# Kernel tuning notes

Hardware: AMD Instinct MI355X
Metric: run time of the kernel (lower is better)

## Reference

```python
import jax, jax.numpy as jnp
import numpy as np

HEAD_DIM = 128
N_HEADS = 16
N_KV_HEADS = 4
ROPE_BASE = 10000.0
TRAIN_SEQ_LEN = 1024


def _rotary_cos_sin(seq_len, rd, base=ROPE_BASE, train_len=TRAIN_SEQ_LEN):
    # NTK-style base scaling when seq_len exceeds training length (matches Rotary.forward)
    if seq_len > train_len:
        scale = seq_len / train_len
        base = base * scale ** (rd / (rd - 2))
    inv_freq = 1.0 / base ** (np.arange(0, rd, 2, dtype=np.float32) / rd)
    freqs = np.outer(np.arange(seq_len, dtype=np.float32), inv_freq)  # [T, rd/2]
    cos = jnp.asarray(np.cos(freqs))[None, :, None, :]  # [1,T,1,rd/2]
    sin = jnp.asarray(np.sin(freqs))[None, :, None, :]
    return cos, sin


def _apply_rotary(x, cos, sin):
    h = x.shape[-1] // 2
    x1, x2 = x[..., :h], x[..., h:]
    return jnp.concatenate((x1 * cos + x2 * sin, -x1 * sin + x2 * cos), axis=-1)


def _rms_norm(x):
    eps = jnp.finfo(x.dtype).eps
    return x * jax.lax.rsqrt(jnp.mean(x * x, axis=-1, keepdims=True) + eps)


def setup_inputs() -> dict:
    key = jax.random.key(0)
    ks = jax.random.split(key, 6)
    B, T, D = 4, 2048, 2048
    x = jax.random.normal(ks[0], (B, T, D), dtype=jnp.float32)
    q_w = jax.random.normal(ks[1], (D, D), dtype=jnp.float32) * 0.02
    k_w = jax.random.normal(ks[2], (N_KV_HEADS * HEAD_DIM, D), dtype=jnp.float32) * 0.02
    v_w = jax.random.normal(ks[3], (N_KV_HEADS * HEAD_DIM, D), dtype=jnp.float32) * 0.02
    out_w = jax.random.normal(ks[4], (D, D), dtype=jnp.float32) * 0.02
    q_gain = jnp.ones((N_HEADS,), dtype=jnp.float32)
    return {"x": x, "q_w": q_w, "k_w": k_w, "v_w": v_w, "out_w": out_w, "q_gain": q_gain}


def reference(x, q_w, k_w, v_w, out_w, q_gain):
    B, T, D = x.shape
    q = (x @ q_w.T).reshape(B, T, N_HEADS, HEAD_DIM)
    k = (x @ k_w.T).reshape(B, T, N_KV_HEADS, HEAD_DIM)
    v = (x @ v_w.T).reshape(B, T, N_KV_HEADS, HEAD_DIM)
    q = _rms_norm(q)
    k = _rms_norm(k)
    cos, sin = _rotary_cos_sin(T, HEAD_DIM)
    q = _apply_rotary(q, cos, sin)
    k = _apply_rotary(k, cos, sin)
    q = q * q_gain[None, None, :, None]
    # GQA: expand kv heads (repeat_interleave semantics)
    rep = N_HEADS // N_KV_HEADS
    k = jnp.repeat(k, rep, axis=2)  # [B,T,H,D]
    v = jnp.repeat(v, rep, axis=2)
    scale = 1.0 / jnp.sqrt(jnp.asarray(HEAD_DIM, dtype=x.dtype))
    scores = jnp.einsum("bthd,bshd->bhts", q, k) * scale  # [B,H,T,T]
    causal = jnp.tril(jnp.ones((T, T), dtype=bool))
    scores = jnp.where(causal[None, None], scores, jnp.asarray(-jnp.inf, dtype=scores.dtype))
    w = jax.nn.softmax(scores, axis=-1)
    y = jnp.einsum("bhts,bshd->bthd", w, v).reshape(B, T, D)
    return y @ out_w.T
```

## Files before the change

### kernel.cpp

```cpp
#include <hip/hip_runtime.h>
#include <hip/hip_bf16.h>
#include <math.h>

#define HEAD_DIM 128
#define NH 16
#define NKV 4
#define BB 4
#define TT 2048
#define DD 2048
#define ROWS (BB*TT)

typedef unsigned short u16;
typedef unsigned int u32;
typedef __attribute__((ext_vector_type(8))) short short8;
typedef __attribute__((ext_vector_type(4))) float f32x4;
typedef __attribute__((ext_vector_type(16))) float f32x16;
typedef __attribute__((ext_vector_type(4))) unsigned short u16x4;

__device__ __forceinline__ float bf2f(u16 u) {
    union { unsigned int i; float f; } v; v.i = ((unsigned int)u) << 16; return v.f;
}
__device__ __forceinline__ u16 f2bf(float f) {
    union { float f; unsigned int i; } v; v.f = f;
    unsigned int r = v.i + 0x7FFFu + ((v.i >> 16) & 1u);
    return (u16)(r >> 16);
}
__device__ __forceinline__ f32x4 mfma16(short8 a, short8 b, f32x4 c) {
    return __builtin_amdgcn_mfma_f32_16x16x32_bf16(a, b, c, 0, 0, 0);
}
__device__ __forceinline__ f32x16 mfma32(short8 a, short8 b, f32x16 c) {
    return __builtin_amdgcn_mfma_f32_32x32x16_bf16(a, b, c, 0, 0, 0);
}
__device__ __forceinline__ f32x16 zero16() {
    f32x16 z;
    #pragma unroll
    for (int i = 0; i < 16; ++i) z[i] = 0.f;
    return z;
}
__device__ __forceinline__ void gload_lds16(const u16* g, u16* l) {
    __builtin_amdgcn_global_load_lds(
        (const __attribute__((address_space(1))) unsigned int*)(const void*)g,
        (__attribute__((address_space(3))) unsigned int*)(void*)l, 16, 0, 0);
}

__global__ __launch_bounds__(256)
void cast_f2b(const float* __restrict__ in, u16* __restrict__ out, int n)
{
    int i = (blockIdx.x * 256 + threadIdx.x) * 4;
    if (i >= n) return;
    float4 v = *(const float4*)(in + i);
    u16x4 o;
    o.x = f2bf(v.x); o.y = f2bf(v.y); o.z = f2bf(v.z); o.w = f2bf(v.w);
    *(u16x4*)(out + i) = o;
}

__global__ __launch_bounds__(256)
void prep_all(const float* __restrict__ x,  const float* __restrict__ qw,
              const float* __restrict__ kw, const float* __restrict__ vw,
              u16* __restrict__ xh, u16* __restrict__ wq, u16* __restrict__ wkv,
              float* __restrict__ cs, float* __restrict__ sn, float base)
{
    const int bid = blockIdx.x, tid = threadIdx.x;
    if (bid < 22528) {
        const float* src; u16* dst; int i4;
        if (bid < 16384)      { src = x;  dst = xh;            i4 = bid; }
        else if (bid < 20480) { src = qw; dst = wq;            i4 = bid - 16384; }
        else if (bid < 21504) { src = kw; dst = wkv;           i4 = bid - 20480; }
        else                  { src = vw; dst = wkv + 1048576; i4 = bid - 21504; }
        int i = (i4 * 256 + tid) * 4;
        float4 v = *(const float4*)(src + i);
        u16x4 o;
        o.x = f2bf(v.x); o.y = f2bf(v.y); o.z = f2bf(v.z); o.w = f2bf(v.w);
        *(u16x4*)(dst + i) = o;
    } else {
        int idx = (bid - 22528) * 256 + tid;
        int t = idx >> 6;
        int d = idx & 63;
        float inv = powf(base, -(float)(2 * d) / 128.0f);
        float f = (float)t * inv;
        cs[idx] = cosf(f);
        sn[idx] = sinf(f);
    }
}

__global__ __launch_bounds__(256)
void rmsrope_qk(const u16* __restrict__ qin, u16* __restrict__ qout,
                const u16* __restrict__ kin, u16* __restrict__ kout,
                const float* __restrict__ cs, const float* __restrict__ sn,
                const float* __restrict__ gain, float pre)
{
    int row  = blockIdx.x * 4 + (threadIdx.x >> 6);
    int lane = threadIdx.x & 63;
    const u16* xin; u16* xout; int heads; int use_gain;
    if (row < 131072) { xin = qin; xout = qout; heads = NH;  use_gain = 1; }
    else { row -= 131072; xin = kin; xout = kout; heads = NKV; use_gain = 0; }

    int h = row % heads;
    int t = (row / heads) % TT;
    int b = row / (heads * TT);
    size_t base = (size_t)row * HEAD_DIM;

    float x1 = bf2f(xin[base + lane]);
    float x2 = bf2f(xin[base + 64 + lane]);
    float ss = x1 * x1 + x2 * x2;
    #pragma unroll
    for (int m = 1; m < 64; m <<= 1) ss += __shfl_xor(ss, m, 64);
    float r = 1.0f / sqrtf(ss * (1.0f / 128.0f) + 1.1920929e-7f);
    x1 *= r; x2 *= r;

    float c = cs[t * 64 + lane];
    float s = sn[t * 64 + lane];
    float o1 =  x1 * c + x2 * s;
    float o2 = -x1 * s + x2 * c;
    float g = use_gain ? gain[h] * pre : 1.0f;
    o1 *= g; o2 *= g;

    size_t obase = ((size_t)(b * heads + h) * TT + t) * HEAD_DIM;
    xout[obase + lane]      = f2bf(o1);
    xout[obase + 64 + lane] = f2bf(o2);
}

__global__ __launch_bounds__(256)
void transpose_v(const u16* __restrict__ vbh, u16* __restrict__ vtb)
{
    __shared__ u16 tile[64][72];
    const int tb = blockIdx.x;
    const int db = blockIdx.y;
    const int z  = blockIdx.z;
    const int tid = threadIdx.x;

    {
        const int r = tid >> 2, cq = tid & 3;
        const u16* src = vbh + ((size_t)(((z >> 2) * TT + tb * 64 + r) * NKV + (z & 3))) * 128
                             + db * 64 + cq * 16;
        short8 s0 = *(const short8*)(src);
        short8 s1 = *(const short8*)(src + 8);
        #pragma unroll
        for (int e = 0; e < 8; ++e) tile[r][cq * 16 + e]     = (u16)s0[e];
        #pragma unroll
        for (int e = 0; e < 8; ++e) tile[r][cq * 16 + 8 + e] = (u16)s1[e];
    }
    __syncthreads();
    {
        const int d = tid >> 2, tq = tid & 3;
        __attribute__((aligned(16))) u16 tmp[16];
        #pragma unroll
        for (int e = 0; e < 16; ++e) {
            int esw = (e & 3) | ((e & 4) << 1) | ((e & 8) >> 1);
            tmp[e] = tile[tq * 16 + esw][d];
        }
        u16* dst = vtb + (((size_t)(z * (TT / 64) + tb) * 128 + (db * 64 + d)) << 6) + tq * 16;
        *(short8*)(dst)     = ((short8*)tmp)[0];
        *(short8*)(dst + 8) = ((short8*)tmp)[1];
    }
}

template<int BN, int OUTMODE>
__global__ __launch_bounds__(512, 2)
void gemm256(const u16* __restrict__ A, const u16* __restrict__ W,
             void* __restrict__ C0, void* __restrict__ C1)
{
    constexpr int WN    = (BN == 256) ? 4 : 2;
    constexpr int MR    = (BN == 256) ? 8 : 4;
    constexpr int WROW  = (BN == 256) ? 128 : 64;
    constexpr int NT    = DD / 64;
    constexpr int NBI   = (BN == 256) ? 4 : 2;
    constexpr int BPR   = BN / 16;

    __shared__ u16 AsL[2 * 128 * 128];
    __shared__ u16 BsL[2 * (BN / 2) * 128];

    const int tid = threadIdx.x;
    const int w = tid >> 6, l = tid & 63;
    const int lq = l & 15, lg = l >> 4;
    const int wmi = (WN == 4) ? (w >> 2) : (w >> 1);
    const int wni = w & (WN - 1);

    int bmi, bni;
    {
        const int bid = blockIdx.x;
        const int wg = (bid & 7) * 32 + (bid >> 3);
        const int st = wg >> 2, wi = wg & 3;
        const int sty = st >> 2, stx = st & 3;
        bmi = sty * 2 + (wi >> 1);
        bni = stx * 2 + (wi & 1);
    }
    const int bm = bmi * 256, bn = bni * BN;

    const int sro = l >> 4;
    const int sch = l & 15;

    f32x4 acc[MR][4];
    #pragma unroll
    for (int m = 0; m < MR; ++m)
        #pragma unroll
        for (int n = 0; n < 4; ++n) acc[m][n] = (f32x4){0.f, 0.f, 0.f, 0.f};

    auto stage = [&](int buf, int t) {
        const size_t ko = (size_t)t * 64;
        u16* Ad = AsL + buf * (128 * 128);
        u16* Bd = BsL + buf * ((BN / 2) * 128);
        #pragma unroll
        for (int j = 0; j < 4; ++j) {
            int rp = w * 16 + j * 4 + sro;
            int cg = sch ^ (rp & 15);
            gload_lds16(A + (size_t)(bm + 2 * rp + (cg >> 3)) * DD + ko + (cg & 7) * 8,
                        Ad + (w * 16 + j * 4) * 128);
        }
        #pragma unroll
        for (int j = 0; j < NBI; ++j) {
            int rp = w * BPR + j * 4 + sro;
            int cg = sch ^ (rp & 15);
            gload_lds16(W + (size_t)(bn + 2 * rp + (cg >> 3)) * DD + ko + (cg & 7) * 8,
                        Bd + (w * BPR + j * 4) * 128);
        }
    };

    stage(0, 0);
    stage(1, 1);
    if constexpr (BN == 256) asm volatile("s_waitcnt vmcnt(8)" ::: "memory");
    else                     asm volatile("s_waitcnt vmcnt(6)" ::: "memory");
    __builtin_amdgcn_s_barrier();
    __builtin_amdgcn_sched_barrier(0);

    const int mh = lq >> 1;
    const int e8 = (lq & 1) << 3;
    for (int t = 0; t < NT; ++t) {
        const int buf = t & 1;
        const u16* Ab = AsL + buf * (128 * 128);
        const u16* Bb = BsL + buf * ((BN / 2) * 128);
        #pragma unroll
        for (int ks = 0; ks < 2; ++ks) {
            short8 af[MR], bf[4];
            #pragma unroll
            for (int m = 0; m < MR; ++m) {
                int rp = wmi * (WROW / 2) + m * 8 + mh;
                af[m] = *(const short8*)(Ab + rp * 128 + (((e8 + ks * 4 + lg) ^ (rp & 15)) << 3));
            }
            #pragma unroll
            for (int n = 0; n < 4; ++n) {
                int rp = wni * 32 + n * 8 + mh;
                bf[n] = *(const short8*)(Bb + rp * 128 + (((e8 + ks * 4 + lg) ^ (rp & 15)) << 3));
            }
            __builtin_amdgcn_s_setprio(1);
            #pragma unroll
            for (int m = 0; m < MR; ++m)
                #pragma unroll
                for (int n = 0; n < 4; ++n)
                    acc[m][n] = mfma16(af[m], bf[n], acc[m][n]);
            __builtin_amdgcn_s_setprio(0);
        }

        if (t + 1 < NT) {
            __builtin_amdgcn_sched_barrier(0);
            __builtin_amdgcn_s_barrier();
            if (t + 2 < NT) {
                stage(buf, t + 2);
                if constexpr (BN == 256) asm volatile("s_waitcnt vmcnt(8)" ::: "memory");
                else                     asm volatile("s_waitcnt vmcnt(6)" ::: "memory");
            } else {
                asm volatile("s_waitcnt vmcnt(0)" ::: "memory");
            }
            __builtin_amdgcn_s_barrier();
            __builtin_amdgcn_sched_barrier(0);
        }
    }

    #pragma unroll
    for (int m = 0; m < MR; ++m) {
        int grow = bm + wmi * WROW + m * 16 + lg * 4;
        #pragma unroll
        for (int n = 0; n < 4; ++n) {
            int col = wni * 64 + n * 16 + lq;
            #pragma unroll
            for (int q = 0; q < 4; ++q) {
                float v = acc[m][n][q];
                if constexpr (OUTMODE == 0) {
                    ((u16*)C0)[(size_t)(grow + q) * 2048 + bn + col] = f2bf(v);
                } else if constexpr (OUTMODE == 2) {
                    ((float*)C0)[(size_t)(grow + q) * 2048 + bn + col] = v;
                } else {
                    int cg = bn + col;
                    if (cg < 512)
                        ((u16*)C0)[(size_t)(grow + q) * 512 + cg] = f2bf(v);
                    else
                        ((u16*)C1)[(size_t)(grow + q) * 512 + (cg - 512)] = f2bf(v);
                }
            }
        }
    }
}

__global__ __launch_bounds__(256, 2)
void attn_mfma(const u16* __restrict__ qg,
               const u16* __restrict__ kg,
               const u16* __restrict__ vtg,
               u16* __restrict__ yg)
{
    __shared__ u16 Ks[2][64 * 128];
    __shared__ u16 Vs[2][64 * 128];

    const int tid = threadIdx.x, wid = tid >> 6, l = tid & 63;
    const int lq = l & 31, hi = l >> 5, hi4 = hi << 2;

    const int bid = blockIdx.x;
    const int xcd  = bid & 7;
    const int s    = bid >> 3;
    const int gsub = s >> 5;
    const int hh   = (s >> 3) & 3;
    const int fold = s & 7;
    const int g    = xcd + (gsub << 3);
    const int b = g >> 2, kvh = g & 3;
    const int h = kvh * 4 + hh;

    const u16* kg_bh = kg + (((size_t)g * TT) << 7);
    const u16* vt_bh = vtg + (size_t)g * (TT / 64) * 8192;
    const u16* q_bh  = qg + (((size_t)(b * NH + h) * TT) << 7);

    const int nta = 2 * fold + 2;
    const int NT  = 34;

    const int sro = l >> 4;
    const int sch = l & 15;

    auto stage = [&](int buf, int kt) {
        #pragma unroll
        for (int i = 0; i < 4; ++i) {
            int kr = wid * 16 + i * 4 + sro;
            int cgk = sch ^ (kr & 15);
            gload_lds16(kg_bh + (((size_t)(kt * 64 + kr)) << 7) + (cgk << 3),
                        &Ks[buf][(wid * 16 + i * 4) << 7]);
            int rp = wid * 16 + i * 4 + sro;
            int cgv = sch ^ (rp & 15);
            gload_lds16(vt_bh + (size_t)kt * 8192 + ((2 * rp + (cgv >> 3)) << 6) + ((cgv & 7) << 3),
                        &Vs[buf][(wid * 16 + i * 4) << 7]);
        }
    };

    stage(0, 0);
    stage(1, 1);
    asm volatile("s_waitcnt vmcnt(8)" ::: "memory");
    __builtin_amdgcn_s_barrier();
    __builtin_amdgcn_sched_barrier(0);

    int step = 0;

    for (int seg = 0; seg < 2; ++seg) {
        const int qblk = seg ? (15 - fold) : fold;
        const int nseg = seg ? (32 - 2 * fold) : nta;
        const int qrow = qblk * 128 + wid * 32 + lq;
        const int diag = (qblk * 128 + wid * 32) >> 6;

        const u16* qptr = q_bh + ((size_t)qrow << 7) + hi * 8;
        short8 qf[8];
        #pragma unroll
        for (int q = 0; q < 8; ++q)
            qf[q] = *(const short8*)(qptr + q * 16);

        f32x16 accO[4];
        #pragma unroll
        for (int d = 0; d < 4; ++d) accO[d] = zero16();
        float m2 = -1e30f, lr = 0.f;

        for (int kt = 0; kt < nseg; ++kt, ++step) {
            const int buf = step & 1;

            if (kt <= diag) {
                const u16* Kc = Ks[buf];
                f32x16 accS0 = zero16(), accS1 = zero16();
                __builtin_amdgcn_s_setprio(1);
                #pragma unroll
                for (int ss = 0; ss < 8; ++ss) {
                    int c = ((2 * ss + hi) ^ (lq & 15)) << 3;
                    short8 kf0 = *(const short8*)(Kc + (lq << 7) + c);
                    accS0 = mfma32(kf0, qf[ss], accS0);
                    short8 kf1 = *(const short8*)(Kc + ((32 + lq) << 7) + c);
                    accS1 = mfma32(kf1, qf[ss], accS1);
                }
                __builtin_amdgcn_s_setprio(0);

                float p[32];
                if (kt == diag) {
                    #pragma unroll
                    for (int r = 0; r < 16; ++r) {
                        int key0 = kt * 64 + (r & 3) + 8 * (r >> 2) + hi4;
                        p[r]      = (key0      > qrow) ? -INFINITY : accS0[r];
                        p[16 + r] = (key0 + 32 > qrow) ? -INFINITY : accS1[r];
                    }
                } else {
                    #pragma unroll
                    for (int r = 0; r < 16; ++r) { p[r] = accS0[r]; p[16 + r] = accS1[r]; }
                }

                float t16[16];
                #pragma unroll
                for (int i = 0; i < 16; ++i) t16[i] = fmaxf(p[i], p[i + 16]);
                #pragma unroll
                for (int i = 0; i < 8; ++i) t16[i] = fmaxf(t16[i], t16[i + 8]);
                #pragma unroll
                for (int i = 0; i < 4; ++i) t16[i] = fmaxf(t16[i], t16[i + 4]);
                float pm = fmaxf(fmaxf(t16[0], t16[1]), fmaxf(t16[2], t16[3]));
                pm = fmaxf(pm, __shfl_xor(pm, 32, 64));

                float mn = m2;
                if (!__all(pm - m2 <= 8.0f)) {
                    mn = fmaxf(m2, pm);
                    float al = exp2f(m2 - mn);
                    lr *= al;
                    #pragma unroll
                    for (int d = 0; d < 4; ++d) accO[d] *= al;
                    m2 = mn;
                }

                #pragma unroll
                for (int r = 0; r < 32; ++r) p[r] = exp2f(p[r] - mn);
                #pragma unroll
                for (int i = 0; i < 16; ++i) t16[i] = p[i] + p[i + 16];
                #pragma unroll
                for (int i = 0; i < 8; ++i) t16[i] += t16[i + 8];
                #pragma unroll
                for (int i = 0; i < 4; ++i) t16[i] += t16[i + 4];
                float rs = (t16[0] + t16[1]) + (t16[2] + t16[3]);
                rs += __shfl_xor(rs, 32, 64);
                lr += rs;

                short8 pfrag[4];
                #pragma unroll
                for (int kb = 0; kb < 2; ++kb)
                    #pragma unroll
                    for (int c = 0; c < 2; ++c) {
                        union { u32 u[4]; short8 s8; } f;
                        #pragma unroll
                        for (int j = 0; j < 4; ++j) {
                            __hip_bfloat162 hb = __float22bfloat162_rn(
                                make_float2(p[kb * 16 + 8 * c + 2 * j],
                                            p[kb * 16 + 8 * c + 2 * j + 1]));
                            f.u[j] = *reinterpret_cast<u32*>(&hb);
                        }
                        pfrag[kb * 2 + c] = f.s8;
                    }

                const u16* Vc = Vs[buf];
                const int rv = lq >> 1;
                const int ev = (lq & 1) << 3;
                #pragma unroll
                for (int d = 0; d < 4; ++d) {
                    const u16* vr8 = Vc + ((d * 16 + rv) << 7);
                    short8 vf0 = *(const short8*)(vr8 + (((ev + 0 + hi) ^ rv) << 3));
                    short8 vf1 = *(const short8*)(vr8 + (((ev + 2 + hi) ^ rv) << 3));
                    short8 vf2 = *(const short8*)(vr8 + (((ev + 4 + hi) ^ rv) << 3));
                    short8 vf3 = *(const short8*)(vr8 + (((ev + 6 + hi) ^ rv) << 3));
                    __builtin_amdgcn_s_setprio(1);
                    accO[d] = mfma32(vf0, pfrag[0], accO[d]);
                    accO[d] = mfma32(vf1, pfrag[1], accO[d]);
                    accO[d] = mfma32(vf2, pfrag[2], accO[d]);
                    accO[d] = mfma32(vf3, pfrag[3], accO[d]);
                    __builtin_amdgcn_s_setprio(0);
                }
            }

            if (step + 1 < NT) {
                __builtin_amdgcn_sched_barrier(0);
                __builtin_amdgcn_s_barrier();
                if (step + 2 < NT) {
                    int tn = step + 2;
                    stage(buf, (tn < nta) ? tn : tn - nta);
                    asm volatile("s_waitcnt vmcnt(8)" ::: "memory");
                } else {
                    asm volatile("s_waitcnt vmcnt(0)" ::: "memory");
                }
                __builtin_amdgcn_s_barrier();
                __builtin_amdgcn_sched_barrier(0);
            }
        }

        float inv = 1.0f / lr;
        u16* yrow = yg + ((size_t)((b * TT + qrow) * NH + h) << 7);
        #pragma unroll
        for (int d = 0; d < 4; ++d)
            #pragma unroll
            for (int r = 0; r < 4; ++r) {
                u16x4 o;
                #pragma unroll
                for (int q = 0; q < 4; ++q) o[q] = f2bf(accO[d][4 * r + q] * inv);
                *(u16x4*)(yrow + d * 32 + 8 * r + hi4) = o;
            }
    }
}

extern "C" void kernel_launch(void* const* d_in, const int* in_sizes, int n_in,
                              void* d_out, int out_size, void* d_ws, size_t ws_size,
                              hipStream_t stream)
{
    const float* x      = (const float*)d_in[0];
    const float* q_w    = (const float*)d_in[1];
    const float* k_w    = (const float*)d_in[2];
    const float* v_w    = (const float*)d_in[3];
    const float* out_w  = (const float*)d_in[4];
    const float* q_gain = (const float*)d_in[5];
    float* out = (float*)d_out;

    char* ws = (char*)d_ws;
    u16* qh   = (u16*)(ws);
    u16* xh   = (u16*)(ws + 33554432ull);
    u16* wqkv = (u16*)(ws + 67108864ull);
    u16* kh   = (u16*)(ws + 79691776ull);
    u16* vbh  = (u16*)(ws + 88080384ull);
    float* cs = (float*)(ws + 96468992ull);
    float* sn = cs + TT * 64;
    u16* wq   = wqkv;
    u16* wkv  = wqkv + 4194304;
    u16* q2   = xh;
    u16* kk   = wqkv;
    u16* vtb  = kh;
    u16* wout = vbh;
    u16* y    = qh;

    dim3 blk(256);

    double base = 10000.0 * pow((double)TT / 1024.0, 128.0 / 126.0);
    prep_all<<<dim3(23040), blk, 0, stream>>>(x, q_w, k_w, v_w, xh, wq, wkv,
                                              cs, sn, (float)base);

    gemm256<256, 0><<<dim3(256), dim3(512), 0, stream>>>(xh, wq, qh, nullptr);
    gemm256<128, 1><<<dim3(256), dim3(512), 0, stream>>>(xh, wkv, kh, vbh);

    const float pre_q = 0.08838834764831845f * 1.4426950408889634f;
    rmsrope_qk<<<dim3(40960), blk, 0, stream>>>(qh, q2, kh, kk, cs, sn, q_gain, pre_q);

    transpose_v<<<dim3(TT / 64, 2, BB * NKV), blk, 0, stream>>>(vbh, vtb);

    cast_f2b<<<dim3(4096), blk, 0, stream>>>(out_w, wout, DD * DD);

    attn_mfma<<<dim3(512), blk, 0, stream>>>(q2, kk, vtb, y);

    gemm256<256, 2><<<dim3(256), dim3(512), 0, stream>>>(y, wout, out, nullptr);
}
```

Before: 346.1 us.

## Fuse RMSNorm, RoPE and gain into Q/K projection GEMM epilogues

Removes the standalone rmsrope_qk kernel and performs RMS normalization, rotary embedding and q-gain scaling inside the QKV GEMM epilogues. Row sums of squares are reduced across warps through a shared-memory buffer, and the rotary partner half is exchanged via LDS in bf16. This drops a full read and write of Q and K plus one launch, at the cost of extra syncs, LDS use and scattered epilogue stores. The partner value is rounded to bf16 before the rotation, which changes rounding slightly.

Measured after the change: 331.0 us. -4.4%, faster.

```diff
diff --git a/kernel.cpp b/kernel.cpp
--- a/kernel.cpp
+++ b/kernel.cpp
@@ -84,43 +84,6 @@
 }
 
 __global__ __launch_bounds__(256)
-void rmsrope_qk(const u16* __restrict__ qin, u16* __restrict__ qout,
-                const u16* __restrict__ kin, u16* __restrict__ kout,
-                const float* __restrict__ cs, const float* __restrict__ sn,
-                const float* __restrict__ gain, float pre)
-{
-    int row  = blockIdx.x * 4 + (threadIdx.x >> 6);
-    int lane = threadIdx.x & 63;
-    const u16* xin; u16* xout; int heads; int use_gain;
-    if (row < 131072) { xin = qin; xout = qout; heads = NH;  use_gain = 1; }
-    else { row -= 131072; xin = kin; xout = kout; heads = NKV; use_gain = 0; }
-
-    int h = row % heads;
-    int t = (row / heads) % TT;
-    int b = row / (heads * TT);
-    size_t base = (size_t)row * HEAD_DIM;
-
-    float x1 = bf2f(xin[base + lane]);
-    float x2 = bf2f(xin[base + 64 + lane]);
-    float ss = x1 * x1 + x2 * x2;
-    #pragma unroll
-    for (int m = 1; m < 64; m <<= 1) ss += __shfl_xor(ss, m, 64);
-    float r = 1.0f / sqrtf(ss * (1.0f / 128.0f) + 1.1920929e-7f);
-    x1 *= r; x2 *= r;
-
-    float c = cs[t * 64 + lane];
-    float s = sn[t * 64 + lane];
-    float o1 =  x1 * c + x2 * s;
-    float o2 = -x1 * s + x2 * c;
-    float g = use_gain ? gain[h] * pre : 1.0f;
-    o1 *= g; o2 *= g;
-
-    size_t obase = ((size_t)(b * heads + h) * TT + t) * HEAD_DIM;
-    xout[obase + lane]      = f2bf(o1);
-    xout[obase + 64 + lane] = f2bf(o2);
-}
-
-__global__ __launch_bounds__(256)
 void transpose_v(const u16* __restrict__ vbh, u16* __restrict__ vtb)
 {
     __shared__ u16 tile[64][72];
@@ -158,7 +121,9 @@
 template<int BN, int OUTMODE>
 __global__ __launch_bounds__(512, 2)
 void gemm256(const u16* __restrict__ A, const u16* __restrict__ W,
-             void* __restrict__ C0, void* __restrict__ C1)
+             void* __restrict__ C0, void* __restrict__ C1,
+             const float* __restrict__ CS, const float* __restrict__ SN,
+             const float* __restrict__ GAIN, float PRE)
 {
     constexpr int WN    = (BN == 256) ? 4 : 2;
     constexpr int MR    = (BN == 256) ? 8 : 4;
@@ -167,8 +132,10 @@
     constexpr int NBI   = (BN == 256) ? 4 : 2;
     constexpr int BPR   = BN / 16;
 
-    __shared__ u16 AsL[2 * 128 * 128];
-    __shared__ u16 BsL[2 * (BN / 2) * 128];
+    __shared__ u16 LDSall[2 * 128 * 128 + 2 * (BN / 2) * 128];
+    __shared__ float Sred[1024];
+    u16* AsL = LDSall;
+    u16* BsL = LDSall + 2 * 128 * 128;
 
     const int tid = threadIdx.x;
     const int w = tid >> 6, l = tid & 63;
@@ -266,25 +233,117 @@
         }
     }
 
-    #pragma unroll
-    for (int m = 0; m < MR; ++m) {
-        int grow = bm + wmi * WROW + m * 16 + lg * 4;
-        #pragma unroll
-        for (int n = 0; n < 4; ++n) {
-            int col = wni * 64 + n * 16 + lq;
-            #pragma unroll
-            for (int q = 0; q < 4; ++q) {
-                float v = acc[m][n][q];
-                if constexpr (OUTMODE == 0) {
-                    ((u16*)C0)[(size_t)(grow + q) * 2048 + bn + col] = f2bf(v);
-                } else if constexpr (OUTMODE == 2) {
-                    ((float*)C0)[(size_t)(grow + q) * 2048 + bn + col] = v;
-                } else {
-                    int cg = bn + col;
-                    if (cg < 512)
-                        ((u16*)C0)[(size_t)(grow + q) * 512 + cg] = f2bf(v);
+    if constexpr (OUTMODE == 2) {
+        #pragma unroll
+        for (int m = 0; m < MR; ++m) {
+            int grow = bm + wmi * WROW + m * 16 + lg * 4;
+            #pragma unroll
+            for (int n = 0; n < 4; ++n) {
+                int col = wni * 64 + n * 16 + lq;
+                #pragma unroll
+                for (int q = 0; q < 4; ++q)
+                    ((float*)C0)[(size_t)(grow + q) * 2048 + bn + col] = acc[m][n][q];
+            }
+        }
+    } else {
+        const int wpar = wni & 1;
+        const int hs   = (OUTMODE == 3) ? (wni >> 1) : 0;
+        const bool isK = (OUTMODE == 3) ? true : (bni < 4);
+        u16* E = LDSall;
+
+        if (isK) {
+            __syncthreads();
+            #pragma unroll
+            for (int m = 0; m < MR; ++m) {
+                f32x4 ps = acc[m][0] * acc[m][0];
+                #pragma unroll
+                for (int n = 1; n < 4; ++n) ps += acc[m][n] * acc[m][n];
+                #pragma unroll
+                for (int q = 0; q < 4; ++q) {
+                    float v = ps[q];
+                    v += __shfl_xor(v, 1, 64);
+                    v += __shfl_xor(v, 2, 64);
+                    v += __shfl_xor(v, 4, 64);
+                    v += __shfl_xor(v, 8, 64);
+                    if (lq == 0) {
+                        int lr = m * 16 + lg * 4 + q;
+                        if constexpr (OUTMODE == 3)
+                            Sred[wmi * 512 + lr * 4 + hs * 2 + wpar] = v;
+                        else
+                            Sred[wmi * 128 + lr * 2 + wpar] = v;
+                    }
+                }
+            }
+            __syncthreads();
+            #pragma unroll
+            for (int m = 0; m < MR; ++m) {
+                f32x4 rs4;
+                #pragma unroll
+                for (int q = 0; q < 4; ++q) {
+                    int lr = m * 16 + lg * 4 + q;
+                    float tot;
+                    if constexpr (OUTMODE == 3)
+                        tot = Sred[wmi * 512 + lr * 4 + hs * 2]
+                            + Sred[wmi * 512 + lr * 4 + hs * 2 + 1];
                     else
-                        ((u16*)C1)[(size_t)(grow + q) * 512 + (cg - 512)] = f2bf(v);
+                        tot = Sred[wmi * 128 + lr * 2]
+                            + Sred[wmi * 128 + lr * 2 + 1];
+                    rs4[q] = 1.0f / sqrtf(tot * (1.0f / 128.0f) + 1.1920929e-7f);
+                }
+                #pragma unroll
+                for (int n = 0; n < 4; ++n) {
+                    acc[m][n] *= rs4;
+                    #pragma unroll
+                    for (int q = 0; q < 4; ++q) {
+                        int lr = m * 16 + lg * 4 + q;
+                        int col = n * 16 + lq;
+                        int eidx = (OUTMODE == 3) ? ((w << 13) + (lr << 6) + col)
+                                                  : ((w << 12) + (lr << 6) + col);
+                        E[eidx] = f2bf(acc[m][n][q]);
+                    }
+                }
+            }
+            __syncthreads();
+            const int pw = w ^ 1;
+            #pragma unroll
+            for (int m = 0; m < MR; ++m)
+                #pragma unroll
+                for (int n = 0; n < 4; ++n)
+                    #pragma unroll
+                    for (int q = 0; q < 4; ++q) {
+                        int lr = m * 16 + lg * 4 + q;
+                        int col = n * 16 + lq;
+                        int eidx = (OUTMODE == 3) ? ((pw << 13) + (lr << 6) + col)
+                                                  : ((pw << 12) + (lr << 6) + col);
+                        float prt = bf2f(E[eidx]);
+                        float mine = acc[m][n][q];
+                        int grow = bm + wmi * WROW + lr;
+                        int tt = grow & 2047, bb = grow >> 11;
+                        float cv = CS[tt * 64 + col];
+                        float sv = SN[tt * 64 + col];
+                        float o;
+                        int d_;
+                        if (wpar == 0) { d_ = col;      o = mine * cv + prt * sv; }
+                        else           { d_ = 64 + col; o = mine * cv - prt * sv; }
+                        if constexpr (OUTMODE == 3) {
+                            int hh_ = (bn >> 7) + hs;
+                            o *= GAIN[hh_] * PRE;
+                            ((u16*)C0)[(((size_t)(bb * NH + hh_) * TT + tt) << 7) + d_] = f2bf(o);
+                        } else {
+                            int kvh_ = bni;
+                            ((u16*)C0)[(((size_t)(bb * NKV + kvh_) * TT + tt) << 7) + d_] = f2bf(o);
+                        }
+                    }
+        } else {
+            #pragma unroll
+            for (int m = 0; m < MR; ++m) {
+                int growb = bm + wmi * WROW + m * 16 + lg * 4;
+                #pragma unroll
+                for (int n = 0; n < 4; ++n) {
+                    int cg = bn + wni * 64 + n * 16 + lq - 512;
+                    #pragma unroll
+                    for (int q = 0; q < 4; ++q)
+                        ((u16*)C1)[(size_t)(growb + q) * 512 + cg] = f2bf(acc[m][n][q]);
                 }
             }
         }
@@ -501,20 +560,18 @@
     float* out = (float*)d_out;
 
     char* ws = (char*)d_ws;
-    u16* qh   = (u16*)(ws);
+    u16* q2   = (u16*)(ws);
     u16* xh   = (u16*)(ws + 33554432ull);
     u16* wqkv = (u16*)(ws + 67108864ull);
-    u16* kh   = (u16*)(ws + 79691776ull);
+    u16* vtb  = (u16*)(ws + 79691776ull);
     u16* vbh  = (u16*)(ws + 88080384ull);
     float* cs = (float*)(ws + 96468992ull);
     float* sn = cs + TT * 64;
     u16* wq   = wqkv;
     u16* wkv  = wqkv + 4194304;
-    u16* q2   = xh;
     u16* kk   = wqkv;
-    u16* vtb  = kh;
     u16* wout = vbh;
-    u16* y    = qh;
+    u16* y    = xh;
 
     dim3 blk(256);
 
@@ -522,11 +579,11 @@
     prep_all<<<dim3(23040), blk, 0, stream>>>(x, q_w, k_w, v_w, xh, wq, wkv,
                                               cs, sn, (float)base);
 
-    gemm256<256, 0><<<dim3(256), dim3(512), 0, stream>>>(xh, wq, qh, nullptr);
-    gemm256<128, 1><<<dim3(256), dim3(512), 0, stream>>>(xh, wkv, kh, vbh);
-
     const float pre_q = 0.08838834764831845f * 1.4426950408889634f;
-    rmsrope_qk<<<dim3(40960), blk, 0, stream>>>(qh, q2, kh, kk, cs, sn, q_gain, pre_q);
+    gemm256<256, 3><<<dim3(256), dim3(512), 0, stream>>>(xh, wq, q2, nullptr,
+                                                         cs, sn, q_gain, pre_q);
+    gemm256<128, 4><<<dim3(256), dim3(512), 0, stream>>>(xh, wkv, kk, vbh,
+                                                         cs, sn, nullptr, 0.f);
 
     transpose_v<<<dim3(TT / 64, 2, BB * NKV), blk, 0, stream>>>(vbh, vtb);
 
@@ -534,5 +591,6 @@
 
     attn_mfma<<<dim3(512), blk, 0, stream>>>(q2, kk, vtb, y);
 
-    gemm256<256, 2><<<dim3(256), dim3(512), 0, stream>>>(y, wout, out, nullptr);
-}
+    gemm256<256, 2><<<dim3(256), dim3(512), 0, stream>>>(y, wout, out, nullptr,
+                                                         nullptr, nullptr, nullptr, 0.f);
+}
```
